# Kernel tuning notes

Measured on AMD Instinct MI355X. Metric: run time of the kernel, lower is better.

Reference implementation:

```python
import jax, jax.numpy as jnp
from jax import lax
import numpy as np

B, CIN, HC, K, REC = 64, 64, 64, 3, 5
MG = 240 // REC  # 48
EPS = 1e-8


def conv2d(x, w, b, pad):
    y = lax.conv_general_dilated(x, w, (1, 1), [(pad, pad), (pad, pad)],
                                 dimension_numbers=('NCHW', 'OIHW', 'NCHW'))
    return y + b[None, :, None, None]


def conv_transpose2d(x, w, b, stride, pad):
    # PyTorch ConvTranspose2d: w is (Cin, Cout, kH, kW)
    k = w.shape[2]
    w_t = jnp.transpose(w[:, :, ::-1, ::-1], (1, 0, 2, 3))  # -> OIHW, flipped
    y = lax.conv_general_dilated(x, w_t, (1, 1),
                                 [(k - 1 - pad, k - 1 - pad)] * 2,
                                 lhs_dilation=(stride, stride),
                                 dimension_numbers=('NCHW', 'OIHW', 'NCHW'))
    return y + b[None, :, None, None]


def leaky(x):
    return jnp.where(x >= 0, x, 0.2 * x)


def setup_inputs() -> dict:
    key = jax.random.key(0)
    ks = jax.random.split(key, 12)
    s = 0.05
    return {
        'x': jax.random.normal(ks[0], (B, CIN, 64, 64), jnp.float32),
        'h': jax.random.normal(ks[1], (B, HC, 64, 64), jnp.float32),
        'c': jax.random.normal(ks[2], (B, HC, 64, 64), jnp.float32),
        'recalled_memory_feature': jax.random.normal(ks[3], (B, REC, MG, 32, 32), jnp.float32),
        'conv_w': jax.random.normal(ks[4], (5 * HC, CIN + HC, K, K), jnp.float32) * s,
        'conv_b': jax.random.normal(ks[5], (5 * HC,), jnp.float32) * s,
        'convc_w': jax.random.normal(ks[6], (MG, HC, 1, 1), jnp.float32) * s,
        'convc_b': jax.random.normal(ks[7], (MG,), jnp.float32) * s,
        'convssm_w': jax.random.normal(ks[8], (MG, MG, 4, 4), jnp.float32) * s,
        'convssm_b': jax.random.normal(ks[9], (MG,), jnp.float32) * s,
        'convfuse_w': jax.random.normal(ks[10], (HC, MG + HC, 1, 1), jnp.float32) * s,
        'convfuse_b': jax.random.normal(ks[11], (HC,), jnp.float32) * s,
    }


def reference(x, h, c, recalled_memory_feature, conv_w, conv_b, convc_w, convc_b,
              convssm_w, convssm_b, convfuse_w, convfuse_b):
    rm = recalled_memory_feature.reshape(B, REC, MG, 32, 32)
    rm_avg = rm.mean(axis=(3, 4))                      # (B, REC, MG)
    q = leaky(conv2d(c, convc_w, convc_b, 0))          # (B, MG, 64, 64)
    q_avg = q.mean(axis=(2, 3))                        # (B, MG)
    # cosine similarity along channel dim, vectorized over (B, REC)
    qn = jnp.maximum(jnp.linalg.norm(q_avg, axis=1, keepdims=True), EPS)   # (B,1)
    mn = jnp.maximum(jnp.linalg.norm(rm_avg, axis=2), EPS)                  # (B,REC)
    cos = jnp.einsum('bm,brm->br', q_avg, rm_avg) / (qn * mn)               # (B,REC)
    attn = jax.nn.softmax(cos, axis=1)                                      # (B,REC)
    mt = jnp.einsum('br,brmhw->bmhw', attn, rm)        # (B, MG, 32, 32)
    mt = leaky(conv_transpose2d(mt, convssm_w, convssm_b, 2, 1))  # (B, MG, 64, 64)

    gates = conv2d(jnp.concatenate((x, h), axis=1), conv_w, conv_b, K // 2)
    i, f, g, o, lam = jnp.split(gates, 5, axis=1)
    i = jax.nn.sigmoid(i)
    f = jax.nn.sigmoid(f)
    o = jax.nn.sigmoid(o)
    g = jnp.tanh(g)
    lam = jax.nn.sigmoid(lam)
    c_new = f * c + i * g
    h_new = o * jnp.tanh(conv2d(jnp.concatenate((c_new, mt), axis=1), convfuse_w, convfuse_b, 0))
    h_out = lam * h_new + (1.0 - lam) * h
    return (h_out, c_new)
```

## Files before the change

kernel.cpp:

```cpp
#include <hip/hip_runtime.h>
#include <hip/hip_bf16.h>
#include <cstdint>

#define HW 4096
#define MGc 48
#define RECc 5

typedef __attribute__((ext_vector_type(8))) short bf16x8;
typedef __attribute__((ext_vector_type(4))) float f32x4;

__device__ __forceinline__ float sigf(float x) { return 1.f / (1.f + expf(-x)); }
__device__ __forceinline__ float leakyf(float x) { return x >= 0.f ? x : 0.2f * x; }
__device__ __forceinline__ unsigned short f2bfu(float f) {
  __hip_bfloat16 b = __float2bfloat16(f);
  return *reinterpret_cast<unsigned short*>(&b);
}
__device__ __forceinline__ float bfu2f(unsigned short u) {
  unsigned v = ((unsigned)u) << 16;
  return __uint_as_float(v);
}
__device__ __forceinline__ void gload_lds16(const void* g, void* l) {
  __builtin_amdgcn_global_load_lds(
      (const __attribute__((address_space(1))) unsigned int*)g,
      (__attribute__((address_space(3))) unsigned int*)l, 16, 0, 0);
}

__global__ __launch_bounds__(256) void k_head(const float* __restrict__ cw,
    __hip_bfloat16* __restrict__ Wp, __hip_bfloat16* __restrict__ Pp,
    const float* __restrict__ xin, const float* __restrict__ hin,
    const float* __restrict__ rm, float* __restrict__ rm_sum,
    const float* __restrict__ c, const float* __restrict__ ccw,
    const float* __restrict__ ccb, float* __restrict__ q_part) {
  __shared__ __align__(16) char smem[16704];
  int bid = blockIdx.x;
  int tid = threadIdx.x;
  if (bid < 1440) {
    int idx = bid * 256 + tid;
    int t = idx / (320 * 128);
    int rem = idx % (320 * 128);
    int ocp = rem / 128, ci = rem % 128;
    int nt = ocp / 80, r2 = ocp % 80, gate = r2 / 16, ml = r2 % 16;
    int oc = gate * 64 + nt * 16 + ml;
    Wp[idx] = __float2bfloat16(cw[((size_t)oc * 128 + ci) * 9 + t]);
  } else if (bid < 2480) {
    int idx = (bid - 1440) * 256 + tid;
    int b = idx / 4160, i = idx % 4160;
    bf16x8* base = reinterpret_cast<bf16x8*>(Pp);
    size_t u;
    if (i < 2112) {
      int r = (i < 1056) ? 0 : 65;
      int j = (i < 1056) ? i : i - 1056;
      u = ((size_t)b * 66 + r) * 1056 + j;
    } else {
      int i2 = i - 2112;
      int row = 1 + (i2 >> 5), k = i2 & 31;
      int px = (k < 16) ? 0 : 65, ci8 = k & 15;
      u = (((size_t)b * 66 + row) * 66 + px) * 16 + ci8;
    }
    base[u] = (bf16x8)0;
  } else if (bid < 10672) {
    float (*t)[65] = (float(*)[65])smem;
    int r = bid - 2480;
    int half = r & 1, y = (r >> 1) & 63, b = r >> 7;
    const float* src = (half ? hin : xin) + (size_t)b * 64 * HW + y * 64;
    #pragma unroll
    for (int it = 0; it < 4; it++) {
      int li = it * 256 + tid;
      int ci = li >> 4, x4 = (li & 15) * 4;
      float4 v = *reinterpret_cast<const float4*>(src + (size_t)ci * HW + x4);
      t[x4][ci] = v.x; t[x4 + 1][ci] = v.y; t[x4 + 2][ci] = v.z; t[x4 + 3][ci] = v.w;
    }
    __syncthreads();
    int x = tid >> 2, c16 = (tid & 3) * 16;
    unsigned short* dst = reinterpret_cast<unsigned short*>(Pp) +
        ((((size_t)b * 66 + y + 1) * 66 + x + 1) * 128 + half * 64 + c16);
    bf16x8 o0, o1;
    #pragma unroll
    for (int j = 0; j < 8; j++) {
      o0[j] = (short)f2bfu(t[x][c16 + j]);
      o1[j] = (short)f2bfu(t[x][c16 + 8 + j]);
    }
    *reinterpret_cast<bf16x8*>(dst) = o0;
    *reinterpret_cast<bf16x8*>(dst + 8) = o1;
  } else if (bid < 26032) {
    float* sred = (float*)smem;
    int row = bid - 10672;
    const float4* p = reinterpret_cast<const float4*>(rm + (size_t)row * 1024);
    float4 v = p[tid];
    float s = v.x + v.y + v.z + v.w;
    #pragma unroll
    for (int off = 32; off; off >>= 1) s += __shfl_down(s, off);
    if ((tid & 63) == 0) sred[tid >> 6] = s;
    __syncthreads();
    if (tid == 0) rm_sum[row] = sred[0] + sred[1] + sred[2] + sred[3];
  } else {
    float* wl = (float*)smem;
    float* bl = wl + MGc * 64;
    float (*red)[MGc] = (float(*)[MGc])(bl + 64);
    int r = bid - 26032;
    int seg = r & 15, b = r >> 4;
    for (int i = tid; i < MGc * 64; i += 256) wl[i] = ccw[i];
    if (tid < MGc) bl[tid] = ccb[tid];
    __syncthreads();
    int px = seg * 256 + tid;
    float acc[MGc];
    #pragma unroll
    for (int m = 0; m < MGc; m++) acc[m] = 0.f;
    const float* cp = c + (size_t)b * 64 * HW + px;
    for (int ci = 0; ci < 64; ci++) {
      float v = cp[(size_t)ci * HW];
      #pragma unroll
      for (int m = 0; m < MGc; m++) acc[m] += wl[m * 64 + ci] * v;
    }
    int lane = tid & 63, wv = tid >> 6;
    #pragma unroll
    for (int m = 0; m < MGc; m++) {
      float t2 = leakyf(acc[m] + bl[m]);
      #pragma unroll
      for (int off = 32; off; off >>= 1) t2 += __shfl_down(t2, off);
      if (lane == 0) red[wv][m] = t2;
    }
    __syncthreads();
    if (tid < MGc) {
      float t2 = red[0][tid] + red[1][tid] + red[2][tid] + red[3][tid];
      q_part[((size_t)b * 16 + seg) * MGc + tid] = t2;
    }
  }
}

__global__ __launch_bounds__(256) void k_mt_pre(const float* __restrict__ rm,
    const float* __restrict__ rm_sum, const float* __restrict__ q_part,
    float* __restrict__ mt_pre) {
  __shared__ float sat[RECc];
  int idx = blockIdx.x * 256 + threadIdx.x;
  int b = idx / (MGc * 1024);
  if (threadIdx.x < 64) {
    int lane = threadIdx.x;
    float q = 0.f;
    if (lane < MGc) {
      float s = 0.f;
      for (int sg = 0; sg < 16; sg++) s += q_part[((size_t)b * 16 + sg) * MGc + lane];
      q = s * (1.f / 4096.f);
    }
    float qs = q * q;
    #pragma unroll
    for (int off = 32; off; off >>= 1) qs += __shfl_xor(qs, off);
    float qn = fmaxf(sqrtf(qs), 1e-8f);
    float cosv[RECc];
    #pragma unroll
    for (int r = 0; r < RECc; r++) {
      float m = 0.f;
      if (lane < MGc) m = rm_sum[((size_t)b * RECc + r) * MGc + lane] * (1.f / 1024.f);
      float d = q * m, ms = m * m;
      #pragma unroll
      for (int off = 32; off; off >>= 1) { d += __shfl_xor(d, off); ms += __shfl_xor(ms, off); }
      float mn = fmaxf(sqrtf(ms), 1e-8f);
      cosv[r] = d / (qn * mn);
    }
    float mx = cosv[0];
    #pragma unroll
    for (int r = 1; r < RECc; r++) mx = fmaxf(mx, cosv[r]);
    float ssum = 0.f;
    #pragma unroll
    for (int r = 0; r < RECc; r++) { cosv[r] = expf(cosv[r] - mx); ssum += cosv[r]; }
    float inv = 1.f / ssum;
    #pragma unroll
    for (int r = 0; r < RECc; r++)
      if (lane == r) sat[r] = cosv[r] * inv;
  }
  __syncthreads();
  int rem = idx - b * (MGc * 1024);
  const float* base = rm + (size_t)b * RECc * MGc * 1024 + rem;
  float v = sat[0] * base[0] + sat[1] * base[MGc * 1024] + sat[2] * base[2 * MGc * 1024]
          + sat[3] * base[3 * MGc * 1024] + sat[4] * base[4 * MGc * 1024];
  mt_pre[idx] = v;
}

__global__ __launch_bounds__(512) void k_ssm(const float* __restrict__ mt_pre,
    const float* __restrict__ w, const float* __restrict__ bias,
    __hip_bfloat16* __restrict__ mt) {
  __shared__ float in_t[12][10][20];
  __shared__ float w_t[12][48][16];
  int b = blockIdx.y;
  int tile = blockIdx.x;
  int y0 = (tile >> 1) * 16, x0 = (tile & 1) * 32;
  int wv = threadIdx.x >> 6, lane = threadIdx.x & 63;
  int co0 = wv * 6;
  int oyl = lane >> 2, xseg = lane & 3;
  int oy = y0 + oyl;
  int iy0 = (y0 >> 1) - 1, ix0 = (x0 >> 1) - 1;
  int kyA = (oy + 1) & 1;
  int iyA = (oy + 1 - kyA) >> 1;
  int rA = iyA - iy0, rB = rA - 1;
  float acc[6][8] = {};
  for (int ch = 0; ch < 4; ch++) {
    int ci0 = ch * 12;
    __syncthreads();
    for (int i = threadIdx.x; i < 12 * 10 * 18; i += 512) {
      int ci = i / 180, rr = (i % 180) / 18, cc2 = i % 18;
      int giy = iy0 + rr, gix = ix0 + cc2;
      float v = 0.f;
      if ((unsigned)giy < 32u && (unsigned)gix < 32u)
        v = mt_pre[(((size_t)b * MGc + ci0 + ci) * 32 + giy) * 32 + gix];
      in_t[ci][rr][cc2] = v;
    }
    for (int i = threadIdx.x; i < 12 * 48 * 16; i += 512)
      (&w_t[0][0][0])[i] = w[ci0 * 768 + i];
    __syncthreads();
    #pragma unroll 1
    for (int ci = 0; ci < 12; ci++) {
      float4 a0 = *reinterpret_cast<const float4*>(&in_t[ci][rA][xseg * 4]);
      float4 a1 = *reinterpret_cast<const float4*>(&in_t[ci][rA][xseg * 4 + 4]);
      float4 b0 = *reinterpret_cast<const float4*>(&in_t[ci][rB][xseg * 4]);
      float4 b1 = *reinterpret_cast<const float4*>(&in_t[ci][rB][xseg * 4 + 4]);
      float vA[6] = {a0.x, a0.y, a0.z, a0.w, a1.x, a1.y};
      float vB[6] = {b0.x, b0.y, b0.z, b0.w, b1.x, b1.y};
      #pragma unroll
      for (int co = 0; co < 6; co++) {
        const float* wp = &w_t[ci][co0 + co][0];
        float4 wA = *reinterpret_cast<const float4*>(wp + kyA * 4);
        float4 wB = *reinterpret_cast<const float4*>(wp + (kyA + 2) * 4);
        #pragma unroll
        for (int j = 0; j < 8; j++) {
          if ((j & 1) == 0) {
            int hi = (j >> 1) + 1, lo = j >> 1;
            acc[co][j] += vA[hi] * wA.y + vA[lo] * wA.w + vB[hi] * wB.y + vB[lo] * wB.w;
          } else {
            int hi = ((j + 1) >> 1) + 1, lo = (j + 1) >> 1;
            acc[co][j] += vA[hi] * wA.x + vA[lo] * wA.z + vB[hi] * wB.x + vB[lo] * wB.z;
          }
        }
      }
    }
  }
  int oxb = x0 + xseg * 8;
  #pragma unroll
  for (int co = 0; co < 6; co++) {
    float bb = bias[co0 + co];
    size_t obase = (((size_t)b * MGc + co0 + co) * 64 + oy) * 64 + oxb;
    #pragma unroll
    for (int j = 0; j < 8; j++)
      mt[obase + j] = __float2bfloat16(leakyf(acc[co][j] + bb));
  }
}

__global__ __launch_bounds__(256) void k_gates_mfma(
    const __hip_bfloat16* __restrict__ Pp, const __hip_bfloat16* __restrict__ Wp,
    const float* __restrict__ c, const float* __restrict__ cb,
    float* __restrict__ c_new, __hip_bfloat16* __restrict__ o_g,
    __hip_bfloat16* __restrict__ lam_g) {
  __shared__ bf16x8 s_in[18 * 4 * 18];
  __shared__ bf16x8 s_w[9 * 4 * 80];
  int orig = blockIdx.y * gridDim.x + blockIdx.x;
  int t_id = (orig & 7) * 512 + (orig >> 3);
  int b = t_id >> 6;
  int r6 = t_id & 63;
  int ytile = r6 >> 4, xtile = (r6 >> 2) & 3, nt = r6 & 3;
  int y0 = ytile * 16, x0 = xtile * 16;
  int tid = threadIdx.x;
  int wv = tid >> 6, lane = tid & 63;
  int lane15 = lane & 15, lq = lane >> 4;

  const char* Pb = (const char*)Pp;
  const char* Wb = (const char*)Wp;

  const char* gin[6]; int din[6]; bool ain[6];
  #pragma unroll
  for (int k = 0; k < 6; k++) {
    int u = wv + 4 * k;
    int e = u * 64 + lane;
    ain[k] = (u < 21) && (e < 1296);
    int ee = (e < 1296) ? e : 0;
    int L = ee / 72, r = ee - L * 72;
    int llq = r / 18, xi = r - llq * 18;
    gin[k] = Pb + ((((size_t)b * 66 + y0 + L) * 66 + (x0 + xi)) * 256) + llq * 16;
    din[k] = ee;
  }
  const char* gw[12]; int dw[12]; bool aw[12];
  #pragma unroll
  for (int k = 0; k < 12; k++) {
    int u = wv + 4 * k;
    aw[k] = (u < 45);
    int uu = (u < 45) ? u : 0;
    int e = uu * 64 + lane;
    int unit = e / 80, ol = e - unit * 80;
    int t = unit >> 2, g = unit & 3;
    gw[k] = Wb + (((size_t)t * 320 + nt * 80 + ol) * 128 + g * 8) * 2;
    dw[k] = e;
  }

  f32x4 acc[4][5];
  #pragma unroll
  for (int i = 0; i < 4; i++)
    #pragma unroll
    for (int j = 0; j < 5; j++) acc[i][j] = (f32x4)0.f;

  #pragma unroll 1
  for (int cc = 0; cc < 4; cc++) {
    __syncthreads();
    int co = cc * 64;
    #pragma unroll
    for (int k = 0; k < 6; k++)
      if (ain[k]) gload_lds16(gin[k] + co, (void*)&s_in[din[k]]);
    #pragma unroll
    for (int k = 0; k < 12; k++)
      if (aw[k]) gload_lds16(gw[k] + co, (void*)&s_w[dw[k]]);
    __syncthreads();

    #pragma unroll
    for (int dx = 0; dx < 3; dx++) {
      bf16x8 af[6];
      #pragma unroll
      for (int r = 0; r < 6; r++)
        af[r] = s_in[((wv * 4 + r) * 4 + lq) * 18 + lane15 + dx];
      #pragma unroll
      for (int ky = 0; ky < 3; ky++) {
        int t = ky * 3 + dx;
        bf16x8 bw[5];
        #pragma unroll
        for (int gg = 0; gg < 5; gg++)
          bw[gg] = s_w[(t * 4 + lq) * 80 + gg * 16 + lane15];
        __builtin_amdgcn_s_setprio(1);
        #pragma unroll
        for (int rr = 0; rr < 4; rr++)
          #pragma unroll
          for (int gg = 0; gg < 5; gg++)
            acc[rr][gg] = __builtin_amdgcn_mfma_f32_16x16x32_bf16(
                af[rr + ky], bw[gg], acc[rr][gg], 0, 0, 0);
        __builtin_amdgcn_s_setprio(0);
      }
    }
  }

  int m_hid = nt * 16 + lane15;
  float bi = cb[m_hid], bff = cb[64 + m_hid], bgg = cb[128 + m_hid],
        bo = cb[192 + m_hid], bl = cb[256 + m_hid];
  int xb = x0 + lq * 4;
  size_t chofs = ((size_t)b * 64 + m_hid) * HW;
  #pragma unroll
  for (int rr = 0; rr < 4; rr++) {
    int y = y0 + wv * 4 + rr;
    size_t pofs = chofs + (size_t)y * 64 + xb;
    f32x4 cold = *reinterpret_cast<const f32x4*>(c + pofs);
    f32x4 cn;
    unsigned short ov[4], lv[4];
    #pragma unroll
    for (int e = 0; e < 4; e++) {
      float i_ = sigf(acc[rr][0][e] + bi);
      float f_ = sigf(acc[rr][1][e] + bff);
      float g_ = tanhf(acc[rr][2][e] + bgg);
      float o_ = sigf(acc[rr][3][e] + bo);
      float l_ = sigf(acc[rr][4][e] + bl);
      cn[e] = f_ * cold[e] + i_ * g_;
      ov[e] = f2bfu(o_);
      lv[e] = f2bfu(l_);
    }
    *reinterpret_cast<f32x4*>(c_new + pofs) = cn;
    ushort4 ovv = {ov[0], ov[1], ov[2], ov[3]};
    ushort4 lvv = {lv[0], lv[1], lv[2], lv[3]};
    *reinterpret_cast<ushort4*>(reinterpret_cast<unsigned short*>(o_g) + pofs) = ovv;
    *reinterpret_cast<ushort4*>(reinterpret_cast<unsigned short*>(lam_g) + pofs) = lvv;
  }
}

__global__ __launch_bounds__(256) void k_fuse(const float* __restrict__ c_new,
    const __hip_bfloat16* __restrict__ mt, const __hip_bfloat16* __restrict__ o_g,
    const __hip_bfloat16* __restrict__ lam_g, const float* __restrict__ h,
    const float* __restrict__ fw, const float* __restrict__ fb,
    float* __restrict__ h_out) {
  __shared__ float wl[112][64];
  int b = blockIdx.y, seg = blockIdx.x;
  for (int i = threadIdx.x; i < 112 * 64; i += 256) {
    int ci = i >> 6, co = i & 63;
    wl[ci][co] = fw[co * 112 + ci];
  }
  __syncthreads();
  int px = seg * 512 + threadIdx.x * 2;
  size_t bofs = (size_t)b * 64 * HW;
  float2 acc[64];
  #pragma unroll
  for (int co = 0; co < 64; co++) { float bv = fb[co]; acc[co].x = bv; acc[co].y = bv; }
  #pragma unroll 1
  for (int ci = 0; ci < 64; ci++) {
    float2 v = *reinterpret_cast<const float2*>(c_new + bofs + (size_t)ci * HW + px);
    #pragma unroll
    for (int c4 = 0; c4 < 16; c4++) {
      float4 w = *reinterpret_cast<const float4*>(&wl[ci][c4 * 4]);
      acc[c4 * 4 + 0].x += w.x * v.x; acc[c4 * 4 + 0].y += w.x * v.y;
      acc[c4 * 4 + 1].x += w.y * v.x; acc[c4 * 4 + 1].y += w.y * v.y;
      acc[c4 * 4 + 2].x += w.z * v.x; acc[c4 * 4 + 2].y += w.z * v.y;
      acc[c4 * 4 + 3].x += w.w * v.x; acc[c4 * 4 + 3].y += w.w * v.y;
    }
  }
  const unsigned short* mtu = reinterpret_cast<const unsigned short*>(mt);
  size_t mtofs = (size_t)b * MGc * HW + px;
  #pragma unroll 1
  for (int ci = 0; ci < 48; ci++) {
    unsigned u = *reinterpret_cast<const unsigned*>(mtu + mtofs + (size_t)ci * HW);
    float vx = bfu2f((unsigned short)(u & 0xffff));
    float vy = bfu2f((unsigned short)(u >> 16));
    #pragma unroll
    for (int c4 = 0; c4 < 16; c4++) {
      float4 w = *reinterpret_cast<const float4*>(&wl[64 + ci][c4 * 4]);
      acc[c4 * 4 + 0].x += w.x * vx; acc[c4 * 4 + 0].y += w.x * vy;
      acc[c4 * 4 + 1].x += w.y * vx; acc[c4 * 4 + 1].y += w.y * vy;
      acc[c4 * 4 + 2].x += w.z * vx; acc[c4 * 4 + 2].y += w.z * vy;
      acc[c4 * 4 + 3].x += w.w * vx; acc[c4 * 4 + 3].y += w.w * vy;
    }
  }
  const unsigned short* ou = reinterpret_cast<const unsigned short*>(o_g);
  const unsigned short* lu = reinterpret_cast<const unsigned short*>(lam_g);
  #pragma unroll
  for (int co = 0; co < 64; co++) {
    size_t ofs = bofs + (size_t)co * HW + px;
    unsigned uo = *reinterpret_cast<const unsigned*>(ou + ofs);
    unsigned ul = *reinterpret_cast<const unsigned*>(lu + ofs);
    float2 hv = *reinterpret_cast<const float2*>(h + ofs);
    float hnx = tanhf(acc[co].x), hny = tanhf(acc[co].y);
    float ox = bfu2f((unsigned short)(uo & 0xffff)), oy = bfu2f((unsigned short)(uo >> 16));
    float lx = bfu2f((unsigned short)(ul & 0xffff)), ly = bfu2f((unsigned short)(ul >> 16));
    float2 r;
    r.x = lx * (ox * hnx) + (1.f - lx) * hv.x;
    r.y = ly * (oy * hny) + (1.f - ly) * hv.y;
    *reinterpret_cast<float2*>(h_out + ofs) = r;
  }
}

extern "C" void kernel_launch(void* const* d_in, const int* in_sizes, int n_in,
                              void* d_out, int out_size, void* d_ws, size_t ws_size,
                              hipStream_t stream) {
  const float* x   = (const float*)d_in[0];
  const float* h   = (const float*)d_in[1];
  const float* c   = (const float*)d_in[2];
  const float* rm  = (const float*)d_in[3];
  const float* cw  = (const float*)d_in[4];
  const float* cb  = (const float*)d_in[5];
  const float* ccw = (const float*)d_in[6];
  const float* ccb = (const float*)d_in[7];
  const float* sw  = (const float*)d_in[8];
  const float* sb  = (const float*)d_in[9];
  const float* fw  = (const float*)d_in[10];
  const float* fb  = (const float*)d_in[11];

  float* h_out = (float*)d_out;
  float* c_new = h_out + (size_t)16777216;

  char* ws = (char*)d_ws;
  float* rm_sum = (float*)(ws + 0);
  float* q_part = (float*)(ws + 65536);
  float* mt_pre = (float*)(ws + 262144);
  __hip_bfloat16* o_g   = (__hip_bfloat16*)(ws + 0);
  __hip_bfloat16* lam_g = (__hip_bfloat16*)(ws + 33554432);
  __hip_bfloat16* mt    = (__hip_bfloat16*)(ws + 67108864);
  __hip_bfloat16* Pp    = (__hip_bfloat16*)(ws + 92274688);
  __hip_bfloat16* Wp    = (__hip_bfloat16*)(ws + 163643392);

  k_head<<<27056, 256, 0, stream>>>(cw, Wp, Pp, x, h, rm, rm_sum, c, ccw, ccb, q_part);
  k_mt_pre<<<12288, 256, 0, stream>>>(rm, rm_sum, q_part, mt_pre);
  k_ssm<<<dim3(8, 64), 512, 0, stream>>>(mt_pre, sw, sb, mt);
  k_gates_mfma<<<dim3(64, 64), 256, 0, stream>>>(Pp, Wp, c, cb, c_new, o_g, lam_g);
  k_fuse<<<dim3(8, 64), 256, 0, stream>>>(c_new, mt, o_g, lam_g, h, fw, fb, h_out);
}
```

Baseline: 655.9 us.

## Rebalance kernel stages: merge mt_pre with packing, co-schedule ssm with gates

The five-kernel pipeline is regrouped into four. The attention reductions run first, then the attention-weighted mt_pre runs alongside weight and input packing, and the transposed-conv ssm blocks share a launch with the gates MFMA kernel. The gates kernel moves to 512 threads with each wave covering two rows instead of four, which lowers register pressure. mt_pre now lives in the h_out buffer, freeing workspace. The aim is fewer launches and better overlap of independent work, at the cost of a larger LDS arena per block and a mixed-role grid.

```diff
diff --git a/kernel.cpp b/kernel.cpp
--- a/kernel.cpp
+++ b/kernel.cpp
@@ -25,25 +25,119 @@
       (__attribute__((address_space(3))) unsigned int*)l, 16, 0, 0);
 }
 
-__global__ __launch_bounds__(256) void k_head(const float* __restrict__ cw,
+__global__ __launch_bounds__(256) void k_att(const float* __restrict__ rm,
+    float* __restrict__ rm_sum, const float* __restrict__ c,
+    const float* __restrict__ ccw, const float* __restrict__ ccb,
+    float* __restrict__ q_part) {
+  __shared__ __align__(16) char smem[13568];
+  int bid = blockIdx.x, tid = threadIdx.x;
+  if (bid < 15360) {
+    float* sred = (float*)smem;
+    int row = bid;
+    const float4* p = reinterpret_cast<const float4*>(rm + (size_t)row * 1024);
+    float4 v = p[tid];
+    float s = v.x + v.y + v.z + v.w;
+    #pragma unroll
+    for (int off = 32; off; off >>= 1) s += __shfl_down(s, off);
+    if ((tid & 63) == 0) sred[tid >> 6] = s;
+    __syncthreads();
+    if (tid == 0) rm_sum[row] = sred[0] + sred[1] + sred[2] + sred[3];
+  } else {
+    float* wl = (float*)smem;
+    float* bl = wl + MGc * 64;
+    float (*red)[MGc] = (float(*)[MGc])(bl + 64);
+    int r = bid - 15360;
+    int seg = r & 15, b = r >> 4;
+    for (int i = tid; i < MGc * 64; i += 256) wl[i] = ccw[i];
+    if (tid < MGc) bl[tid] = ccb[tid];
+    __syncthreads();
+    int px = seg * 256 + tid;
+    float acc[MGc];
+    #pragma unroll
+    for (int m = 0; m < MGc; m++) acc[m] = 0.f;
+    const float* cp = c + (size_t)b * 64 * HW + px;
+    for (int ci = 0; ci < 64; ci++) {
+      float v = cp[(size_t)ci * HW];
+      #pragma unroll
+      for (int m = 0; m < MGc; m++) acc[m] += wl[m * 64 + ci] * v;
+    }
+    int lane = tid & 63, wv = tid >> 6;
+    #pragma unroll
+    for (int m = 0; m < MGc; m++) {
+      float t2 = leakyf(acc[m] + bl[m]);
+      #pragma unroll
+      for (int off = 32; off; off >>= 1) t2 += __shfl_down(t2, off);
+      if (lane == 0) red[wv][m] = t2;
+    }
+    __syncthreads();
+    if (tid < MGc) {
+      float t2 = red[0][tid] + red[1][tid] + red[2][tid] + red[3][tid];
+      q_part[((size_t)b * 16 + seg) * MGc + tid] = t2;
+    }
+  }
+}
+
+__global__ __launch_bounds__(256) void k_mid(const float* __restrict__ rm,
+    const float* __restrict__ rm_sum, const float* __restrict__ q_part,
+    float* __restrict__ mt_pre, const float* __restrict__ cw,
     __hip_bfloat16* __restrict__ Wp, __hip_bfloat16* __restrict__ Pp,
-    const float* __restrict__ xin, const float* __restrict__ hin,
-    const float* __restrict__ rm, float* __restrict__ rm_sum,
-    const float* __restrict__ c, const float* __restrict__ ccw,
-    const float* __restrict__ ccb, float* __restrict__ q_part) {
+    const float* __restrict__ xin, const float* __restrict__ hin) {
   __shared__ __align__(16) char smem[16704];
-  int bid = blockIdx.x;
-  int tid = threadIdx.x;
-  if (bid < 1440) {
+  int bid = blockIdx.x, tid = threadIdx.x;
+  if (bid < 12288) {
+    float* sat = (float*)smem;
     int idx = bid * 256 + tid;
+    int b = idx / (MGc * 1024);
+    if (tid < 64) {
+      int lane = tid;
+      float q = 0.f;
+      if (lane < MGc) {
+        float s = 0.f;
+        for (int sg = 0; sg < 16; sg++) s += q_part[((size_t)b * 16 + sg) * MGc + lane];
+        q = s * (1.f / 4096.f);
+      }
+      float qs = q * q;
+      #pragma unroll
+      for (int off = 32; off; off >>= 1) qs += __shfl_xor(qs, off);
+      float qn = fmaxf(sqrtf(qs), 1e-8f);
+      float cosv[RECc];
+      #pragma unroll
+      for (int r = 0; r < RECc; r++) {
+        float m = 0.f;
+        if (lane < MGc) m = rm_sum[((size_t)b * RECc + r) * MGc + lane] * (1.f / 1024.f);
+        float d = q * m, ms = m * m;
+        #pragma unroll
+        for (int off = 32; off; off >>= 1) { d += __shfl_xor(d, off); ms += __shfl_xor(ms, off); }
+        float mn = fmaxf(sqrtf(ms), 1e-8f);
+        cosv[r] = d / (qn * mn);
+      }
+      float mx = cosv[0];
+      #pragma unroll
+      for (int r = 1; r < RECc; r++) mx = fmaxf(mx, cosv[r]);
+      float ssum = 0.f;
+      #pragma unroll
+      for (int r = 0; r < RECc; r++) { cosv[r] = expf(cosv[r] - mx); ssum += cosv[r]; }
+      float inv = 1.f / ssum;
+      #pragma unroll
+      for (int r = 0; r < RECc; r++)
+        if (lane == r) sat[r] = cosv[r] * inv;
+    }
+    __syncthreads();
+    int rem = idx - b * (MGc * 1024);
+    const float* base = rm + (size_t)b * RECc * MGc * 1024 + rem;
+    float v = sat[0] * base[0] + sat[1] * base[MGc * 1024] + sat[2] * base[2 * MGc * 1024]
+            + sat[3] * base[3 * MGc * 1024] + sat[4] * base[4 * MGc * 1024];
+    mt_pre[idx] = v;
+  } else if (bid < 13728) {
+    int idx = (bid - 12288) * 256 + tid;
     int t = idx / (320 * 128);
     int rem = idx % (320 * 128);
     int ocp = rem / 128, ci = rem % 128;
     int nt = ocp / 80, r2 = ocp % 80, gate = r2 / 16, ml = r2 % 16;
     int oc = gate * 64 + nt * 16 + ml;
     Wp[idx] = __float2bfloat16(cw[((size_t)oc * 128 + ci) * 9 + t]);
-  } else if (bid < 2480) {
-    int idx = (bid - 1440) * 256 + tid;
+  } else if (bid < 14768) {
+    int idx = (bid - 13728) * 256 + tid;
     int b = idx / 4160, i = idx % 4160;
     bf16x8* base = reinterpret_cast<bf16x8*>(Pp);
     size_t u;
@@ -58,9 +152,9 @@
       u = (((size_t)b * 66 + row) * 66 + px) * 16 + ci8;
     }
     base[u] = (bf16x8)0;
-  } else if (bid < 10672) {
+  } else {
     float (*t)[65] = (float(*)[65])smem;
-    int r = bid - 2480;
+    int r = bid - 14768;
     int half = r & 1, y = (r >> 1) & 63, b = r >> 7;
     const float* src = (half ? hin : xin) + (size_t)b * 64 * HW + y * 64;
     #pragma unroll
@@ -82,284 +176,193 @@
     }
     *reinterpret_cast<bf16x8*>(dst) = o0;
     *reinterpret_cast<bf16x8*>(dst + 8) = o1;
-  } else if (bid < 26032) {
-    float* sred = (float*)smem;
-    int row = bid - 10672;
-    const float4* p = reinterpret_cast<const float4*>(rm + (size_t)row * 1024);
-    float4 v = p[tid];
-    float s = v.x + v.y + v.z + v.w;
-    #pragma unroll
-    for (int off = 32; off; off >>= 1) s += __shfl_down(s, off);
-    if ((tid & 63) == 0) sred[tid >> 6] = s;
-    __syncthreads();
-    if (tid == 0) rm_sum[row] = sred[0] + sred[1] + sred[2] + sred[3];
-  } else {
-    float* wl = (float*)smem;
-    float* bl = wl + MGc * 64;
-    float (*red)[MGc] = (float(*)[MGc])(bl + 64);
-    int r = bid - 26032;
-    int seg = r & 15, b = r >> 4;
-    for (int i = tid; i < MGc * 64; i += 256) wl[i] = ccw[i];
-    if (tid < MGc) bl[tid] = ccb[tid];
-    __syncthreads();
-    int px = seg * 256 + tid;
-    float acc[MGc];
-    #pragma unroll
-    for (int m = 0; m < MGc; m++) acc[m] = 0.f;
-    const float* cp = c + (size_t)b * 64 * HW + px;
-    for (int ci = 0; ci < 64; ci++) {
-      float v = cp[(size_t)ci * HW];
-      #pragma unroll
-      for (int m = 0; m < MGc; m++) acc[m] += wl[m * 64 + ci] * v;
-    }
-    int lane = tid & 63, wv = tid >> 6;
-    #pragma unroll
-    for (int m = 0; m < MGc; m++) {
-      float t2 = leakyf(acc[m] + bl[m]);
-      #pragma unroll
-      for (int off = 32; off; off >>= 1) t2 += __shfl_down(t2, off);
-      if (lane == 0) red[wv][m] = t2;
-    }
-    __syncthreads();
-    if (tid < MGc) {
-      float t2 = red[0][tid] + red[1][tid] + red[2][tid] + red[3][tid];
-      q_part[((size_t)b * 16 + seg) * MGc + tid] = t2;
-    }
-  }
-}
-
-__global__ __launch_bounds__(256) void k_mt_pre(const float* __restrict__ rm,
-    const float* __restrict__ rm_sum, const float* __restrict__ q_part,
-    float* __restrict__ mt_pre) {
-  __shared__ float sat[RECc];
-  int idx = blockIdx.x * 256 + threadIdx.x;
-  int b = idx / (MGc * 1024);
-  if (threadIdx.x < 64) {
-    int lane = threadIdx.x;
-    float q = 0.f;
-    if (lane < MGc) {
-      float s = 0.f;
-      for (int sg = 0; sg < 16; sg++) s += q_part[((size_t)b * 16 + sg) * MGc + lane];
-      q = s * (1.f / 4096.f);
-    }
-    float qs = q * q;
-    #pragma unroll
-    for (int off = 32; off; off >>= 1) qs += __shfl_xor(qs, off);
-    float qn = fmaxf(sqrtf(qs), 1e-8f);
-    float cosv[RECc];
-    #pragma unroll
-    for (int r = 0; r < RECc; r++) {
-      float m = 0.f;
-      if (lane < MGc) m = rm_sum[((size_t)b * RECc + r) * MGc + lane] * (1.f / 1024.f);
-      float d = q * m, ms = m * m;
-      #pragma unroll
-      for (int off = 32; off; off >>= 1) { d += __shfl_xor(d, off); ms += __shfl_xor(ms, off); }
-      float mn = fmaxf(sqrtf(ms), 1e-8f);
-      cosv[r] = d / (qn * mn);
-    }
-    float mx = cosv[0];
-    #pragma unroll
-    for (int r = 1; r < RECc; r++) mx = fmaxf(mx, cosv[r]);
-    float ssum = 0.f;
-    #pragma unroll
-    for (int r = 0; r < RECc; r++) { cosv[r] = expf(cosv[r] - mx); ssum += cosv[r]; }
-    float inv = 1.f / ssum;
-    #pragma unroll
-    for (int r = 0; r < RECc; r++)
-      if (lane == r) sat[r] = cosv[r] * inv;
-  }
-  __syncthreads();
-  int rem = idx - b * (MGc * 1024);
-  const float* base = rm + (size_t)b * RECc * MGc * 1024 + rem;
-  float v = sat[0] * base[0] + sat[1] * base[MGc * 1024] + sat[2] * base[2 * MGc * 1024]
-          + sat[3] * base[3 * MGc * 1024] + sat[4] * base[4 * MGc * 1024];
-  mt_pre[idx] = v;
-}
-
-__global__ __launch_bounds__(512) void k_ssm(const float* __restrict__ mt_pre,
-    const float* __restrict__ w, const float* __restrict__ bias,
-    __hip_bfloat16* __restrict__ mt) {
-  __shared__ float in_t[12][10][20];
-  __shared__ float w_t[12][48][16];
-  int b = blockIdx.y;
-  int tile = blockIdx.x;
-  int y0 = (tile >> 1) * 16, x0 = (tile & 1) * 32;
-  int wv = threadIdx.x >> 6, lane = threadIdx.x & 63;
-  int co0 = wv * 6;
-  int oyl = lane >> 2, xseg = lane & 3;
-  int oy = y0 + oyl;
-  int iy0 = (y0 >> 1) - 1, ix0 = (x0 >> 1) - 1;
-  int kyA = (oy + 1) & 1;
-  int iyA = (oy + 1 - kyA) >> 1;
-  int rA = iyA - iy0, rB = rA - 1;
-  float acc[6][8] = {};
-  for (int ch = 0; ch < 4; ch++) {
-    int ci0 = ch * 12;
-    __syncthreads();
-    for (int i = threadIdx.x; i < 12 * 10 * 18; i += 512) {
-      int ci = i / 180, rr = (i % 180) / 18, cc2 = i % 18;
-      int giy = iy0 + rr, gix = ix0 + cc2;
-      float v = 0.f;
-      if ((unsigned)giy < 32u && (unsigned)gix < 32u)
-        v = mt_pre[(((size_t)b * MGc + ci0 + ci) * 32 + giy) * 32 + gix];
-      in_t[ci][rr][cc2] = v;
-    }
-    for (int i = threadIdx.x; i < 12 * 48 * 16; i += 512)
-      (&w_t[0][0][0])[i] = w[ci0 * 768 + i];
-    __syncthreads();
-    #pragma unroll 1
-    for (int ci = 0; ci < 12; ci++) {
-      float4 a0 = *reinterpret_cast<const float4*>(&in_t[ci][rA][xseg * 4]);
-      float4 a1 = *reinterpret_cast<const float4*>(&in_t[ci][rA][xseg * 4 + 4]);
-      float4 b0 = *reinterpret_cast<const float4*>(&in_t[ci][rB][xseg * 4]);
-      float4 b1 = *reinterpret_cast<const float4*>(&in_t[ci][rB][xseg * 4 + 4]);
-      float vA[6] = {a0.x, a0.y, a0.z, a0.w, a1.x, a1.y};
-      float vB[6] = {b0.x, b0.y, b0.z, b0.w, b1.x, b1.y};
-      #pragma unroll
-      for (int co = 0; co < 6; co++) {
-        const float* wp = &w_t[ci][co0 + co][0];
-        float4 wA = *reinterpret_cast<const float4*>(wp + kyA * 4);
-        float4 wB = *reinterpret_cast<const float4*>(wp + (kyA + 2) * 4);
-        #pragma unroll
-        for (int j = 0; j < 8; j++) {
-          if ((j & 1) == 0) {
-            int hi = (j >> 1) + 1, lo = j >> 1;
-            acc[co][j] += vA[hi] * wA.y + vA[lo] * wA.w + vB[hi] * wB.y + vB[lo] * wB.w;
-          } else {
-            int hi = ((j + 1) >> 1) + 1, lo = (j + 1) >> 1;
-            acc[co][j] += vA[hi] * wA.x + vA[lo] * wA.z + vB[hi] * wB.x + vB[lo] * wB.z;
-          }
-        }
-      }
-    }
-  }
-  int oxb = x0 + xseg * 8;
-  #pragma unroll
-  for (int co = 0; co < 6; co++) {
-    float bb = bias[co0 + co];
-    size_t obase = (((size_t)b * MGc + co0 + co) * 64 + oy) * 64 + oxb;
-    #pragma unroll
-    for (int j = 0; j < 8; j++)
-      mt[obase + j] = __float2bfloat16(leakyf(acc[co][j] + bb));
-  }
-}
-
-__global__ __launch_bounds__(256) void k_gates_mfma(
+  }
+}
+
+__global__ __launch_bounds__(512, 4) void k_main(
     const __hip_bfloat16* __restrict__ Pp, const __hip_bfloat16* __restrict__ Wp,
     const float* __restrict__ c, const float* __restrict__ cb,
     float* __restrict__ c_new, __hip_bfloat16* __restrict__ o_g,
-    __hip_bfloat16* __restrict__ lam_g) {
-  __shared__ bf16x8 s_in[18 * 4 * 18];
-  __shared__ bf16x8 s_w[9 * 4 * 80];
-  int orig = blockIdx.y * gridDim.x + blockIdx.x;
-  int t_id = (orig & 7) * 512 + (orig >> 3);
-  int b = t_id >> 6;
-  int r6 = t_id & 63;
-  int ytile = r6 >> 4, xtile = (r6 >> 2) & 3, nt = r6 & 3;
-  int y0 = ytile * 16, x0 = xtile * 16;
-  int tid = threadIdx.x;
-  int wv = tid >> 6, lane = tid & 63;
-  int lane15 = lane & 15, lq = lane >> 4;
-
-  const char* Pb = (const char*)Pp;
-  const char* Wb = (const char*)Wp;
-
-  const char* gin[6]; int din[6]; bool ain[6];
-  #pragma unroll
-  for (int k = 0; k < 6; k++) {
-    int u = wv + 4 * k;
-    int e = u * 64 + lane;
-    ain[k] = (u < 21) && (e < 1296);
-    int ee = (e < 1296) ? e : 0;
-    int L = ee / 72, r = ee - L * 72;
-    int llq = r / 18, xi = r - llq * 18;
-    gin[k] = Pb + ((((size_t)b * 66 + y0 + L) * 66 + (x0 + xi)) * 256) + llq * 16;
-    din[k] = ee;
-  }
-  const char* gw[12]; int dw[12]; bool aw[12];
-  #pragma unroll
-  for (int k = 0; k < 12; k++) {
-    int u = wv + 4 * k;
-    aw[k] = (u < 45);
-    int uu = (u < 45) ? u : 0;
-    int e = uu * 64 + lane;
-    int unit = e / 80, ol = e - unit * 80;
-    int t = unit >> 2, g = unit & 3;
-    gw[k] = Wb + (((size_t)t * 320 + nt * 80 + ol) * 128 + g * 8) * 2;
-    dw[k] = e;
-  }
-
-  f32x4 acc[4][5];
-  #pragma unroll
-  for (int i = 0; i < 4; i++)
-    #pragma unroll
-    for (int j = 0; j < 5; j++) acc[i][j] = (f32x4)0.f;
-
-  #pragma unroll 1
-  for (int cc = 0; cc < 4; cc++) {
-    __syncthreads();
-    int co = cc * 64;
-    #pragma unroll
-    for (int k = 0; k < 6; k++)
-      if (ain[k]) gload_lds16(gin[k] + co, (void*)&s_in[din[k]]);
-    #pragma unroll
-    for (int k = 0; k < 12; k++)
-      if (aw[k]) gload_lds16(gw[k] + co, (void*)&s_w[dw[k]]);
-    __syncthreads();
-
-    #pragma unroll
-    for (int dx = 0; dx < 3; dx++) {
-      bf16x8 af[6];
-      #pragma unroll
-      for (int r = 0; r < 6; r++)
-        af[r] = s_in[((wv * 4 + r) * 4 + lq) * 18 + lane15 + dx];
-      #pragma unroll
-      for (int ky = 0; ky < 3; ky++) {
-        int t = ky * 3 + dx;
-        bf16x8 bw[5];
+    __hip_bfloat16* __restrict__ lam_g,
+    const float* __restrict__ mt_pre, const float* __restrict__ sw,
+    const float* __restrict__ sb, __hip_bfloat16* __restrict__ mt) {
+  __shared__ __align__(16) char arena[66816];
+  int bid = blockIdx.x, tid = threadIdx.x;
+  if (bid < 4096) {
+    bf16x8* s_in = (bf16x8*)arena;
+    bf16x8* s_w  = (bf16x8*)(arena + 20736);
+    int t_id = (bid & 7) * 512 + (bid >> 3);
+    int b = t_id >> 6;
+    int r6 = t_id & 63;
+    int ytile = r6 >> 4, xtile = (r6 >> 2) & 3, nt = r6 & 3;
+    int y0 = ytile * 16, x0 = xtile * 16;
+    int wv = tid >> 6, lane = tid & 63;
+    int lane15 = lane & 15, lq = lane >> 4;
+
+    const char* Pb = (const char*)Pp;
+    const char* Wb = (const char*)Wp;
+
+    const char* gin[3]; int din[3]; bool ain[3];
+    #pragma unroll
+    for (int k = 0; k < 3; k++) {
+      int u = wv + 8 * k;
+      int e = u * 64 + lane;
+      ain[k] = (e < 1296);
+      int ee = (e < 1296) ? e : 0;
+      int L = ee / 72, r = ee - L * 72;
+      int llq = r / 18, xi = r - llq * 18;
+      gin[k] = Pb + ((((size_t)b * 66 + y0 + L) * 66 + (x0 + xi)) * 256) + llq * 16;
+      din[k] = ee;
+    }
+    const char* gw[6]; int dw[6]; bool aw[6];
+    #pragma unroll
+    for (int k = 0; k < 6; k++) {
+      int u = wv + 8 * k;
+      aw[k] = (u < 45);
+      int uu = aw[k] ? u : 0;
+      int e = uu * 64 + lane;
+      int unit = e / 80, ol = e - unit * 80;
+      int t = unit >> 2, g = unit & 3;
+      gw[k] = Wb + (((size_t)t * 320 + nt * 80 + ol) * 128 + g * 8) * 2;
+      dw[k] = e;
+    }
+
+    f32x4 acc[2][5];
+    #pragma unroll
+    for (int i = 0; i < 2; i++)
+      #pragma unroll
+      for (int j = 0; j < 5; j++) acc[i][j] = (f32x4)0.f;
+
+    #pragma unroll 1
+    for (int cc = 0; cc < 4; cc++) {
+      __syncthreads();
+      int co = cc * 64;
+      #pragma unroll
+      for (int k = 0; k < 3; k++)
+        if (ain[k]) gload_lds16(gin[k] + co, (void*)&s_in[din[k]]);
+      #pragma unroll
+      for (int k = 0; k < 6; k++)
+        if (aw[k]) gload_lds16(gw[k] + co, (void*)&s_w[dw[k]]);
+      __syncthreads();
+
+      #pragma unroll
+      for (int dx = 0; dx < 3; dx++) {
+        bf16x8 af[4];
         #pragma unroll
-        for (int gg = 0; gg < 5; gg++)
-          bw[gg] = s_w[(t * 4 + lq) * 80 + gg * 16 + lane15];
-        __builtin_amdgcn_s_setprio(1);
+        for (int r = 0; r < 4; r++)
+          af[r] = s_in[((wv * 2 + r) * 4 + lq) * 18 + lane15 + dx];
         #pragma unroll
-        for (int rr = 0; rr < 4; rr++)
+        for (int ky = 0; ky < 3; ky++) {
+          int t = ky * 3 + dx;
+          bf16x8 bw[5];
           #pragma unroll
           for (int gg = 0; gg < 5; gg++)
-            acc[rr][gg] = __builtin_amdgcn_mfma_f32_16x16x32_bf16(
-                af[rr + ky], bw[gg], acc[rr][gg], 0, 0, 0);
-        __builtin_amdgcn_s_setprio(0);
-      }
-    }
-  }
-
-  int m_hid = nt * 16 + lane15;
-  float bi = cb[m_hid], bff = cb[64 + m_hid], bgg = cb[128 + m_hid],
-        bo = cb[192 + m_hid], bl = cb[256 + m_hid];
-  int xb = x0 + lq * 4;
-  size_t chofs = ((size_t)b * 64 + m_hid) * HW;
-  #pragma unroll
-  for (int rr = 0; rr < 4; rr++) {
-    int y = y0 + wv * 4 + rr;
-    size_t pofs = chofs + (size_t)y * 64 + xb;
-    f32x4 cold = *reinterpret_cast<const f32x4*>(c + pofs);
-    f32x4 cn;
-    unsigned short ov[4], lv[4];
-    #pragma unroll
-    for (int e = 0; e < 4; e++) {
-      float i_ = sigf(acc[rr][0][e] + bi);
-      float f_ = sigf(acc[rr][1][e] + bff);
-      float g_ = tanhf(acc[rr][2][e] + bgg);
-      float o_ = sigf(acc[rr][3][e] + bo);
-      float l_ = sigf(acc[rr][4][e] + bl);
-      cn[e] = f_ * cold[e] + i_ * g_;
-      ov[e] = f2bfu(o_);
-      lv[e] = f2bfu(l_);
-    }
-    *reinterpret_cast<f32x4*>(c_new + pofs) = cn;
-    ushort4 ovv = {ov[0], ov[1], ov[2], ov[3]};
-    ushort4 lvv = {lv[0], lv[1], lv[2], lv[3]};
-    *reinterpret_cast<ushort4*>(reinterpret_cast<unsigned short*>(o_g) + pofs) = ovv;
-    *reinterpret_cast<ushort4*>(reinterpret_cast<unsigned short*>(lam_g) + pofs) = lvv;
+            bw[gg] = s_w[(t * 4 + lq) * 80 + gg * 16 + lane15];
+          __builtin_amdgcn_s_setprio(1);
+          #pragma unroll
+          for (int rr = 0; rr < 2; rr++)
+            #pragma unroll
+            for (int gg = 0; gg < 5; gg++)
+              acc[rr][gg] = __builtin_amdgcn_mfma_f32_16x16x32_bf16(
+                  af[rr + ky], bw[gg], acc[rr][gg], 0, 0, 0);
+          __builtin_amdgcn_s_setprio(0);
+        }
+      }
+    }
+
+    int m_hid = nt * 16 + lane15;
+    float bi = cb[m_hid], bff = cb[64 + m_hid], bgg = cb[128 + m_hid],
+          bo = cb[192 + m_hid], bl = cb[256 + m_hid];
+    int xb = x0 + lq * 4;
+    size_t chofs = ((size_t)b * 64 + m_hid) * HW;
+    #pragma unroll
+    for (int rr = 0; rr < 2; rr++) {
+      int y = y0 + wv * 2 + rr;
+      size_t pofs = chofs + (size_t)y * 64 + xb;
+      f32x4 cold = *reinterpret_cast<const f32x4*>(c + pofs);
+      f32x4 cn;
+      unsigned short ov[4], lv[4];
+      #pragma unroll
+      for (int e = 0; e < 4; e++) {
+        float i_ = sigf(acc[rr][0][e] + bi);
+        float f_ = sigf(acc[rr][1][e] + bff);
+        float g_ = tanhf(acc[rr][2][e] + bgg);
+        float o_ = sigf(acc[rr][3][e] + bo);
+        float l_ = sigf(acc[rr][4][e] + bl);
+        cn[e] = f_ * cold[e] + i_ * g_;
+        ov[e] = f2bfu(o_);
+        lv[e] = f2bfu(l_);
+      }
+      *reinterpret_cast<f32x4*>(c_new + pofs) = cn;
+      ushort4 ovv = {ov[0], ov[1], ov[2], ov[3]};
+      ushort4 lvv = {lv[0], lv[1], lv[2], lv[3]};
+      *reinterpret_cast<ushort4*>(reinterpret_cast<unsigned short*>(o_g) + pofs) = ovv;
+      *reinterpret_cast<ushort4*>(reinterpret_cast<unsigned short*>(lam_g) + pofs) = lvv;
+    }
+  } else {
+    float (*in_t)[10][20] = (float(*)[10][20])arena;
+    float (*w_t)[48][16]  = (float(*)[48][16])(arena + 9600);
+    int sbid = bid - 4096;
+    int tile = sbid & 7, b = sbid >> 3;
+    int y0 = (tile >> 1) * 16, x0 = (tile & 1) * 32;
+    int wv = tid >> 6, lane = tid & 63;
+    int co0 = wv * 6;
+    int oyl = lane >> 2, xseg = lane & 3;
+    int oy = y0 + oyl;
+    int iy0 = (y0 >> 1) - 1, ix0 = (x0 >> 1) - 1;
+    int kyA = (oy + 1) & 1;
+    int iyA = (oy + 1 - kyA) >> 1;
+    int rA = iyA - iy0, rB = rA - 1;
+    float acc[6][8] = {};
+    for (int ch = 0; ch < 4; ch++) {
+      int ci0 = ch * 12;
+      __syncthreads();
+      for (int i = tid; i < 12 * 10 * 18; i += 512) {
+        int ci = i / 180, rr = (i % 180) / 18, cc2 = i % 18;
+        int giy = iy0 + rr, gix = ix0 + cc2;
+        float v = 0.f;
+        if ((unsigned)giy < 32u && (unsigned)gix < 32u)
+          v = mt_pre[(((size_t)b * MGc + ci0 + ci) * 32 + giy) * 32 + gix];
+        in_t[ci][rr][cc2] = v;
+      }
+      for (int i = tid; i < 12 * 48 * 16; i += 512)
+        (&w_t[0][0][0])[i] = sw[ci0 * 768 + i];
+      __syncthreads();
+      #pragma unroll 1
+      for (int ci = 0; ci < 12; ci++) {
+        float4 a0 = *reinterpret_cast<const float4*>(&in_t[ci][rA][xseg * 4]);
+        float4 a1 = *reinterpret_cast<const float4*>(&in_t[ci][rA][xseg * 4 + 4]);
+        float4 b0 = *reinterpret_cast<const float4*>(&in_t[ci][rB][xseg * 4]);
+        float4 b1 = *reinterpret_cast<const float4*>(&in_t[ci][rB][xseg * 4 + 4]);
+        float vA[6] = {a0.x, a0.y, a0.z, a0.w, a1.x, a1.y};
+        float vB[6] = {b0.x, b0.y, b0.z, b0.w, b1.x, b1.y};
+        #pragma unroll
+        for (int co = 0; co < 6; co++) {
+          const float* wp = &w_t[ci][co0 + co][0];
+          float4 wA = *reinterpret_cast<const float4*>(wp + kyA * 4);
+          float4 wB = *reinterpret_cast<const float4*>(wp + (kyA + 2) * 4);
+          #pragma unroll
+          for (int j = 0; j < 8; j++) {
+            if ((j & 1) == 0) {
+              int hi = (j >> 1) + 1, lo = j >> 1;
+              acc[co][j] += vA[hi] * wA.y + vA[lo] * wA.w + vB[hi] * wB.y + vB[lo] * wB.w;
+            } else {
+              int hi = ((j + 1) >> 1) + 1, lo = (j + 1) >> 1;
+              acc[co][j] += vA[hi] * wA.x + vA[lo] * wA.z + vB[hi] * wB.x + vB[lo] * wB.z;
+            }
+          }
+        }
+      }
+    }
+    int oxb = x0 + xseg * 8;
+    #pragma unroll
+    for (int co = 0; co < 6; co++) {
+      float bb = sb[co0 + co];
+      size_t obase = (((size_t)b * MGc + co0 + co) * 64 + oy) * 64 + oxb;
+      #pragma unroll
+      for (int j = 0; j < 8; j++)
+        mt[obase + j] = __float2bfloat16(leakyf(acc[co][j] + bb));
+    }
   }
 }
 
@@ -448,16 +451,15 @@
   char* ws = (char*)d_ws;
   float* rm_sum = (float*)(ws + 0);
   float* q_part = (float*)(ws + 65536);
-  float* mt_pre = (float*)(ws + 262144);
   __hip_bfloat16* o_g   = (__hip_bfloat16*)(ws + 0);
   __hip_bfloat16* lam_g = (__hip_bfloat16*)(ws + 33554432);
   __hip_bfloat16* mt    = (__hip_bfloat16*)(ws + 67108864);
   __hip_bfloat16* Pp    = (__hip_bfloat16*)(ws + 92274688);
   __hip_bfloat16* Wp    = (__hip_bfloat16*)(ws + 163643392);
-
-  k_head<<<27056, 256, 0, stream>>>(cw, Wp, Pp, x, h, rm, rm_sum, c, ccw, ccb, q_part);
-  k_mt_pre<<<12288, 256, 0, stream>>>(rm, rm_sum, q_part, mt_pre);
-  k_ssm<<<dim3(8, 64), 512, 0, stream>>>(mt_pre, sw, sb, mt);
-  k_gates_mfma<<<dim3(64, 64), 256, 0, stream>>>(Pp, Wp, c, cb, c_new, o_g, lam_g);
+  float* mt_pre = h_out;
+
+  k_att<<<16384, 256, 0, stream>>>(rm, rm_sum, c, ccw, ccb, q_part);
+  k_mid<<<22960, 256, 0, stream>>>(rm, rm_sum, q_part, mt_pre, cw, Wp, Pp, x, h);
+  k_main<<<4608, 512, 0, stream>>>(Pp, Wp, c, cb, c_new, o_g, lam_g, mt_pre, sw, sb, mt);
   k_fuse<<<dim3(8, 64), 256, 0, stream>>>(c_new, mt, o_g, lam_g, h, fw, fb, h_out);
 }
```

New measurement: 660.8 us. About the same (+0.7%).
